# Optimization experiments

Measured on AMD Instinct MI355X. Metric: run time of the kernel, lower is better.

The kernel has to match this reference:

```python
import jax, jax.numpy as jnp
import numpy as np
from jax import lax

B, L = 16, 2048
D_TOK, D_TIS = 256, 64
D_MODEL = D_TOK + D_TIS          # 320
EXPAND = 2
D_INNER = EXPAND * D_MODEL       # 640
D_STATE = 16
D_CONV = 4
DT_RANK = (D_MODEL + 15) // 16   # 20 (ceil(d_model/16), Mamba default)
H_OUT = 128
VOCAB = 65                       # len(CODON_MAP_DNA)+1
N_TISSUES = 30
MAX_NORM = 2.0


def _embed_maxnorm(W, idx):
    # torch nn.Embedding(max_norm=2): looked-up rows are renormalized to norm<=2
    e = W[idx]
    n = jnp.linalg.norm(e, axis=-1, keepdims=True)
    return e * jnp.minimum(1.0, MAX_NORM / jnp.maximum(n, 1e-12))


def setup_inputs() -> dict:
    key = jax.random.key(0)
    ks = jax.random.split(key, 18)
    s = 0.02
    seq_W = jax.random.normal(ks[3], (VOCAB, D_TOK), dtype=jnp.float32)
    seq_W = seq_W.at[0].set(0.0)  # padding_idx=0
    A_log = jnp.log(jnp.broadcast_to(jnp.arange(1, D_STATE + 1, dtype=jnp.float32), (D_INNER, D_STATE)))
    return {
        "rna_data_pad": jax.random.randint(ks[0], (B, L), 0, VOCAB).astype(jnp.int32),
        "tissue_id": jax.random.randint(ks[1], (B,), 0, N_TISSUES).astype(jnp.int32),
        "seq_lengths": jax.random.randint(ks[2], (B,), 1, L + 1).astype(jnp.int32),
        "seq_W": seq_W,
        "tissue_W": jax.random.normal(ks[4], (N_TISSUES, D_TIS), dtype=jnp.float32),
        "in_proj_W": jax.random.normal(ks[5], (2 * D_INNER, D_MODEL), dtype=jnp.float32) * s,
        "conv_w": jax.random.normal(ks[6], (D_INNER, 1, D_CONV), dtype=jnp.float32) * s,
        "conv_b": jnp.zeros((D_INNER,), dtype=jnp.float32),
        "x_proj_W": jax.random.normal(ks[7], (DT_RANK + 2 * D_STATE, D_INNER), dtype=jnp.float32) * s,
        "dt_proj_W": jax.random.normal(ks[8], (D_INNER, DT_RANK), dtype=jnp.float32) * s,
        "dt_proj_b": jax.random.uniform(ks[9], (D_INNER,), minval=-4.0, maxval=-2.0),
        "A_log": A_log,
        "D_skip": jnp.ones((D_INNER,), dtype=jnp.float32),
        "out_proj_W": jax.random.normal(ks[10], (D_MODEL, D_INNER), dtype=jnp.float32) * s,
        "p1_W": jax.random.normal(ks[11], (H_OUT, D_MODEL), dtype=jnp.float32) * s,
        "p1_b": jnp.zeros((H_OUT,), dtype=jnp.float32),
        "p2_W": jax.random.normal(ks[12], (1, H_OUT), dtype=jnp.float32) * s,
        "p2_b": jnp.zeros((1,), dtype=jnp.float32),
    }


def reference(rna_data_pad, tissue_id, seq_lengths, seq_W, tissue_W, in_proj_W,
              conv_w, conv_b, x_proj_W, dt_proj_W, dt_proj_b, A_log, D_skip,
              out_proj_W, p1_W, p1_b, p2_W, p2_b):
    b, l = rna_data_pad.shape
    # embeddings + tissue broadcast + mask
    seq_emb = _embed_maxnorm(seq_W, rna_data_pad)            # [B,L,D_TOK]
    tis_emb = _embed_maxnorm(tissue_W, tissue_id)            # [B,D_TIS]
    tis_exp = jnp.broadcast_to(tis_emb[:, None, :], (b, l, tis_emb.shape[-1]))
    x = jnp.concatenate([seq_emb, tis_exp], axis=-1)          # [B,L,D_MODEL]
    x = x * (rna_data_pad != 0)[..., None]
    # Mamba block
    xz = x @ in_proj_W.T                                      # [B,L,2*D_INNER]
    xm, z = jnp.split(xz, 2, axis=-1)
    xt = xm.transpose(0, 2, 1)                                # [B,D_INNER,L]
    conv = lax.conv_general_dilated(
        xt, conv_w, window_strides=(1,), padding=[(D_CONV - 1, 0)],
        feature_group_count=D_INNER,
        dimension_numbers=("NCH", "OIH", "NCH")) + conv_b[None, :, None]
    xm = jax.nn.silu(conv).transpose(0, 2, 1)                 # [B,L,D_INNER]
    x_dbl = xm @ x_proj_W.T                                   # [B,L,DT_RANK+2*D_STATE]
    dt, Bm, Cm = jnp.split(x_dbl, [DT_RANK, DT_RANK + D_STATE], axis=-1)
    delta = jax.nn.softplus(dt @ dt_proj_W.T + dt_proj_b)     # [B,L,D_INNER]
    A = -jnp.exp(A_log)                                       # [D_INNER,D_STATE]
    # selective scan over time
    xs = (delta.transpose(1, 0, 2), Bm.transpose(1, 0, 2),
          Cm.transpose(1, 0, 2), xm.transpose(1, 0, 2))
    h0 = jnp.zeros((b, D_INNER, D_STATE), dtype=xm.dtype)

    def step(h, t):
        dl, bt, ct, ut = t                                    # [B,di],[B,ds],[B,ds],[B,di]
        dA = jnp.exp(dl[:, :, None] * A)                      # [B,di,ds]
        dBu = (dl * ut)[:, :, None] * bt[:, None, :]          # [B,di,ds]
        h = dA * h + dBu
        y = jnp.einsum("bds,bs->bd", h, ct)
        return h, y

    _, ys = lax.scan(step, h0, xs)                            # ys: [L,B,D_INNER]
    y = ys.transpose(1, 0, 2) + xm * D_skip
    y = y * jax.nn.silu(z)
    out = y @ out_proj_W.T                                    # [B,L,D_MODEL]
    # gather last valid timestep
    out_last = out[jnp.arange(b), seq_lengths - 1]            # [B,D_MODEL]
    h1 = jax.nn.relu(out_last @ p1_W.T + p1_b)
    return h1 @ p2_W.T + p2_b                                 # [B,1]
```

## Files before the change

### kernel.cpp

```cpp
#include <hip/hip_runtime.h>
#include <hip/hip_bf16.h>
#include <math.h>

#define B_      16
#define L_      2048
#define D_MODEL 320
#define D_INNER 640
#define D_STATE 16
#define DT_RANK 20
#define H_OUT   128
#define VOCAB   65
#define N_TIS   30
#define TT      8
#define ST      64
#define NCHUNK  16
#define CHLEN   (L_/NCHUNK)

static constexpr size_t OFF_MSEQ  = 0;
static constexpr size_t OFF_MTIS  = OFF_MSEQ + VOCAB*1280;
static constexpr size_t OFF_YSCAN = OFF_MTIS + N_TIS*1280;
static constexpr size_t OFF_CLAST = OFF_YSCAN + B_*D_INNER;
static constexpr size_t OFF_XD20  = OFF_CLAST + B_*16;
static constexpr size_t OFF_BBAR  = OFF_XD20 + (size_t)B_*L_*20;
static constexpr size_t OFF_PC    = OFF_BBAR + (size_t)B_*D_STATE*L_;
static constexpr size_t OFF_SC    = OFF_PC + (size_t)B_*NCHUNK*40*256;

__device__ __forceinline__ float fast_rcp(float x) { return __builtin_amdgcn_rcpf(x); }
__device__ __forceinline__ float silu_f(float x) { return x * fast_rcp(1.0f + __expf(-x)); }

__global__ __launch_bounds__(256) void k_mbuild(
    const float* __restrict__ seqW, const float* __restrict__ tisW,
    const float* __restrict__ inW, float* __restrict__ ws)
{
    __shared__ float a_l[256];
    __shared__ float red[4];
    int v = blockIdx.x, tid = threadIdx.x;
    int K, wofs; const float* src; float* dstM;
    if (v < VOCAB) { K = 256; wofs = 0;   src = seqW + (size_t)v*256;        dstM = ws + OFF_MSEQ + (size_t)v*1280; }
    else           { K = 64;  wofs = 256; src = tisW + (size_t)(v-VOCAB)*64; dstM = ws + OFF_MTIS + (size_t)(v-VOCAB)*1280; }
    float x = (tid < K) ? src[tid] : 0.0f;
    float ss = x * x;
    #pragma unroll
    for (int o = 32; o; o >>= 1) ss += __shfl_xor(ss, o);
    if ((tid & 63) == 0) red[tid >> 6] = ss;
    __syncthreads();
    float tot = red[0] + red[1] + red[2] + red[3];
    float scale = fminf(1.0f, 2.0f / fmaxf(sqrtf(tot), 1e-12f));
    a_l[tid] = (tid < K) ? x * scale : 0.0f;
    __syncthreads();

    int wv = tid >> 6, l = tid & 63;
    float4 a4 = ((const float4*)a_l)[l];
    int j0 = blockIdx.y * 256 + wv * 64;
    bool lane_on = (4*l < K);
    for (int jj = 0; jj < 64; jj += 4) {
        float p[4];
        #pragma unroll
        for (int u = 0; u < 4; ++u) {
            float pv = 0.0f;
            if (lane_on) {
                const float4 w4 = *(const float4*)(inW + (size_t)(j0 + jj + u)*320 + wofs + 4*l);
                pv = a4.x*w4.x + a4.y*w4.y + a4.z*w4.z + a4.w*w4.w;
            }
            p[u] = pv;
        }
        float ta, tb;
        ta=__shfl_xor(p[0],1); tb=__shfl_xor(p[1],1); p[0]=(l&1)?(p[1]+tb):(p[0]+ta);
        ta=__shfl_xor(p[2],1); tb=__shfl_xor(p[3],1); p[2]=(l&1)?(p[3]+tb):(p[2]+ta);
        ta=__shfl_xor(p[0],2); tb=__shfl_xor(p[2],2); p[0]=(l&2)?(p[2]+tb):(p[0]+ta);
        p[0]+=__shfl_xor(p[0],4);  p[0]+=__shfl_xor(p[0],8);
        p[0]+=__shfl_xor(p[0],16); p[0]+=__shfl_xor(p[0],32);
        if (l < 4) dstM[j0 + jj + l] = p[0];
    }
}

__global__ __launch_bounds__(256) void k_xdbl(
    const int* __restrict__ idx, const int* __restrict__ tissue_id,
    const int* __restrict__ seq_lengths,
    const float* __restrict__ conv_w, const float* __restrict__ conv_b,
    const float* __restrict__ xW, float* __restrict__ ws)
{
    __shared__ float u_l[TT*641];
    __shared__ float xd_l[TT*36];
    __shared__ int   idx_l[TT+3];
    int b = blockIdx.y;
    int t0 = blockIdx.x * TT;
    int t_last = seq_lengths[b] - 1;
    if (t0 > t_last) return;
    int tid = threadIdx.x;
    const float* Mseq = ws + OFF_MSEQ;
    const float* Mtis = ws + OFF_MTIS;
    int tis = tissue_id[b];
    if (tid < TT+3) {
        int t = t0 - 3 + tid;
        idx_l[tid] = (t >= 0) ? idx[b*L_ + t] : 0;
    }
    __syncthreads();

    for (int d = tid; d < D_INNER; d += 256) {
        float w0 = conv_w[d*4+0], w1 = conv_w[d*4+1], w2 = conv_w[d*4+2], w3 = conv_w[d*4+3];
        float cb = conv_b[d];
        float mt = Mtis[(size_t)tis*1280 + d];
        float xzv[TT+3];
        #pragma unroll
        for (int k = 0; k < TT+3; ++k) {
            unsigned ro = (unsigned)idx_l[k] * 1280u;
            xzv[k] = ro ? (Mseq[ro + (unsigned)d] + mt) : 0.0f;
        }
        #pragma unroll
        for (int t = 0; t < TT; ++t) {
            float c = cb;
            c = fmaf(w0, xzv[t+0], c);
            c = fmaf(w1, xzv[t+1], c);
            c = fmaf(w2, xzv[t+2], c);
            c = fmaf(w3, xzv[t+3], c);
            u_l[t*641 + d] = silu_f(c);
        }
    }
    __syncthreads();

    {
        int w = tid >> 6, l = tid & 63;
        float wreg[9][10];
        #pragma unroll
        for (int kk = 0; kk < 9; ++kk) {
            const float* xr = xW + (size_t)(w + 4*kk)*D_INNER + l;
            #pragma unroll
            for (int i = 0; i < 10; ++i) wreg[kk][i] = xr[64*i];
        }
        for (int t = 0; t < TT; ++t) {
            float p[9];
            #pragma unroll
            for (int kk = 0; kk < 9; ++kk) p[kk] = 0.f;
            #pragma unroll
            for (int i = 0; i < 10; ++i) {
                float ui = u_l[t*641 + l + 64*i];
                #pragma unroll
                for (int kk = 0; kk < 9; ++kk) p[kk] = fmaf(wreg[kk][i], ui, p[kk]);
            }
            {
                float ta, tb;
                ta=__shfl_xor(p[0],1); tb=__shfl_xor(p[1],1); p[0]=(l&1)?(p[1]+tb):(p[0]+ta);
                ta=__shfl_xor(p[2],1); tb=__shfl_xor(p[3],1); p[2]=(l&1)?(p[3]+tb):(p[2]+ta);
                ta=__shfl_xor(p[4],1); tb=__shfl_xor(p[5],1); p[4]=(l&1)?(p[5]+tb):(p[4]+ta);
                ta=__shfl_xor(p[6],1); tb=__shfl_xor(p[7],1); p[6]=(l&1)?(p[7]+tb):(p[6]+ta);
                p[8]+=__shfl_xor(p[8],1);
                ta=__shfl_xor(p[0],2); tb=__shfl_xor(p[2],2); p[0]=(l&2)?(p[2]+tb):(p[0]+ta);
                ta=__shfl_xor(p[4],2); tb=__shfl_xor(p[6],2); p[4]=(l&2)?(p[6]+tb):(p[4]+ta);
                p[8]+=__shfl_xor(p[8],2);
                ta=__shfl_xor(p[0],4); tb=__shfl_xor(p[4],4); p[0]=(l&4)?(p[4]+tb):(p[0]+ta);
                p[8]+=__shfl_xor(p[8],4);
                ta=__shfl_xor(p[0],8); tb=__shfl_xor(p[8],8); p[0]=(l&8)?(p[8]+tb):(p[0]+ta);
                p[0]+=__shfl_xor(p[0],16);
                p[0]+=__shfl_xor(p[0],32);
            }
            if (l < 9) xd_l[t*36 + w + 4*l] = p[0];
        }
        if (t_last < t0 + TT) {
            int tl = t_last - t0;
            float pc[4];
            #pragma unroll
            for (int k = 0; k < 4; ++k) pc[k] = 0.f;
            #pragma unroll
            for (int i = 0; i < 10; ++i) {
                float ui = u_l[tl*641 + l + 64*i];
                #pragma unroll
                for (int k = 0; k < 4; ++k)
                    pc[k] = fmaf(xW[(size_t)(36 + w + 4*k)*D_INNER + l + 64*i], ui, pc[k]);
            }
            #pragma unroll
            for (int o = 32; o; o >>= 1) {
                #pragma unroll
                for (int k = 0; k < 4; ++k) pc[k] += __shfl_xor(pc[k], o);
            }
            if (l == 0) {
                #pragma unroll
                for (int k = 0; k < 4; ++k) ws[OFF_CLAST + b*16 + w + 4*k] = pc[k];
            }
        }
    }
    __syncthreads();

    {
        int nt = min(TT, t_last - t0 + 1);
        int cnt = nt * 20;
        float* dst = ws + OFF_XD20 + ((size_t)b*L_ + t0)*20;
        for (int o = tid; o < cnt; o += 256) {
            int t = o / 20, r = o - t*20;
            dst[o] = xd_l[t*36 + r];
        }
        int cntB = nt * 16;
        if (tid < cntB) {
            int s, tt;
            if (nt == TT) { s = tid >> 3; tt = tid & 7; }
            else          { s = tid / nt; tt = tid - s*nt; }
            ws[OFF_BBAR + ((size_t)b*D_STATE + s)*L_ + t0 + tt] = xd_l[tt*36 + 20 + s];
        }
    }
}

__global__ __launch_bounds__(256) void k_scanc(
    const int* __restrict__ idx, const int* __restrict__ tissue_id,
    const int* __restrict__ seq_lengths,
    const float* __restrict__ conv_w, const float* __restrict__ conv_b,
    const float* __restrict__ dtW, const float* __restrict__ dtb,
    const float* __restrict__ A_log, float* __restrict__ ws)
{
    __shared__ float xd_t[ST*20];
    __shared__ float dl_t[16*68];
    __shared__ float du_t[16*68];
    __shared__ float Bb_t[16*68];
    __shared__ float sdred[16*17];
    __shared__ int   idx_t[ST+3];

    int dg = blockIdx.x, b = blockIdx.y, c = blockIdx.z;
    int t_last = seq_lengths[b] - 1;
    int t_begin = c * CHLEN;
    if (t_begin > t_last) return;
    int t_end = min(t_begin + CHLEN - 1, t_last);
    int tid = threadIdx.x;
    int dl = tid >> 4, s = tid & 15;
    int dd = tid & 15, tg = tid >> 4;
    int d_own = dg*16 + dd;
    unsigned dco = (unsigned)d_own;
    int tis = tissue_id[b];
    const float* Mseq = ws + OFF_MSEQ;

    float dtw_r[20];
    #pragma unroll
    for (int i = 0; i < 20; i += 4) {
        float4 w4 = *(const float4*)(dtW + d_own*20 + i);
        dtw_r[i] = w4.x; dtw_r[i+1] = w4.y; dtw_r[i+2] = w4.z; dtw_r[i+3] = w4.w;
    }
    float4 cw4 = *(const float4*)(conv_w + d_own*4);
    float  cb  = conv_b[d_own];
    float  dtb_v = dtb[d_own];
    float  mt  = ws[OFF_MTIS + (size_t)tis*1280 + d_own];
    float As = -__expf(A_log[(dg*16 + dl)*D_STATE + s]) * 1.44269504089f;

    float h = 0.0f;
    float sdp = 0.0f;
    for (int t0 = t_begin; t0 <= t_end; t0 += ST) {
        int nt = min(ST, t_end - t0 + 1);
        if (tid < ST+3) {
            int t = t0 - 3 + tid;
            idx_t[tid] = (t >= 0 && t < L_) ? idx[b*L_ + t] : 0;
        }
        {
            const float4* src = (const float4*)(ws + OFF_XD20 + ((size_t)b*L_ + t0)*20);
            float4* dst = (float4*)xd_t;
            int cnt4 = nt * 5;
            for (int o = tid; o < cnt4; o += 256) dst[o] = src[o];
        }
        {
            int lr = tid >> 4, c4 = (tid & 15) * 4;
            if (c4 < nt)
                *(float4*)(Bb_t + lr*68 + c4) =
                    *(const float4*)(ws + OFF_BBAR + ((size_t)b*D_STATE + lr)*L_ + t0 + c4);
        }
        __syncthreads();

        {
            int ttb = tg * 4;
            if (ttb < nt) {
                float xz[7];
                #pragma unroll
                for (int k = 0; k < 7; ++k) {
                    unsigned ro = (unsigned)idx_t[ttb + k] * 1280u;
                    xz[k] = ro ? (Mseq[ro + dco] + mt) : 0.0f;
                }
                float dl4[4], du4[4];
                bool full = (ttb + 3 < nt);
                #pragma unroll
                for (int j = 0; j < 4; ++j) {
                    int tt = ttb + j;
                    if (full || tt < nt) {
                        float cc = cb;
                        cc = fmaf(cw4.x, xz[j+0], cc);
                        cc = fmaf(cw4.y, xz[j+1], cc);
                        cc = fmaf(cw4.z, xz[j+2], cc);
                        cc = fmaf(cw4.w, xz[j+3], cc);
                        float u = silu_f(cc);
                        const float* xr = xd_t + tt*20;
                        float x = dtb_v;
                        #pragma unroll
                        for (int r = 0; r < 20; r += 4) {
                            float4 x4 = *(const float4*)(xr + r);
                            x = fmaf(x4.x, dtw_r[r+0], x);
                            x = fmaf(x4.y, dtw_r[r+1], x);
                            x = fmaf(x4.z, dtw_r[r+2], x);
                            x = fmaf(x4.w, dtw_r[r+3], x);
                        }
                        float e = __expf(-fabsf(x));
                        float sp = fmaxf(x, 0.0f) + __logf(1.0f + e);
                        dl4[j] = sp;
                        du4[j] = sp * u;
                        sdp += sp;
                    } else { dl4[j] = 0.f; du4[j] = 0.f; }
                }
                if (full) {
                    *(float4*)(dl_t + dd*68 + ttb) = make_float4(dl4[0], dl4[1], dl4[2], dl4[3]);
                    *(float4*)(du_t + dd*68 + ttb) = make_float4(du4[0], du4[1], du4[2], du4[3]);
                } else {
                    for (int j = 0; j < 4 && ttb + j < nt; ++j) {
                        dl_t[dd*68 + ttb + j] = dl4[j];
                        du_t[dd*68 + ttb + j] = du4[j];
                    }
                }
            }
        }
        __syncthreads();

        {
            int q4 = nt >> 2;
            #pragma unroll 8
            for (int q = 0; q < q4; ++q) {
                float4 d4 = *(const float4*)(dl_t + dl*68 + 4*q);
                float4 u4 = *(const float4*)(du_t + dl*68 + 4*q);
                float4 b4 = *(const float4*)(Bb_t + s*68 + 4*q);
                float e0 = exp2f(d4.x*As), e1 = exp2f(d4.y*As);
                float e2 = exp2f(d4.z*As), e3 = exp2f(d4.w*As);
                float c0 = u4.x*b4.x, c1 = u4.y*b4.y;
                float c2 = u4.z*b4.z, c3 = u4.w*b4.w;
                h = fmaf(e0, h, c0); h = fmaf(e1, h, c1);
                h = fmaf(e2, h, c2); h = fmaf(e3, h, c3);
            }
            for (int tt = q4*4; tt < nt; ++tt) {
                float dlt = dl_t[dl*68 + tt];
                h = fmaf(exp2f(dlt * As), h, du_t[dl*68 + tt] * Bb_t[s*68 + tt]);
            }
        }
        __syncthreads();
    }
    sdred[tg*17 + dd] = sdp;
    __syncthreads();
    float sd = 0.0f;
    #pragma unroll
    for (int g = 0; g < 16; ++g) sd += sdred[g*17 + dl];
    float P = exp2f(As * sd);
    size_t base = (((size_t)b*NCHUNK + c)*40 + dg)*256 + tid;
    ws[OFF_PC + base] = P;
    ws[OFF_SC + base] = h;
}

__global__ __launch_bounds__(256) void k_comb(const int* __restrict__ seq_lengths,
                                              float* __restrict__ ws)
{
    int b = blockIdx.y, dg = blockIdx.x;
    int tid = threadIdx.x;
    int dl = tid >> 4, s = tid & 15;
    int t_last = seq_lengths[b] - 1;
    int ncv = t_last / CHLEN + 1;
    float h = 0.0f;
    for (int c = 0; c < ncv; ++c) {
        size_t base = (((size_t)b*NCHUNK + c)*40 + dg)*256 + tid;
        h = fmaf(ws[OFF_PC + base], h, ws[OFF_SC + base]);
    }
    float v = h * ws[OFF_CLAST + b*16 + s];
    v += __shfl_xor(v, 1); v += __shfl_xor(v, 2);
    v += __shfl_xor(v, 4); v += __shfl_xor(v, 8);
    if (s == 0) ws[OFF_YSCAN + (size_t)b*D_INNER + dg*16 + dl] = v;
}

__global__ __launch_bounds__(320) void k_final(
    const int* __restrict__ idx, const int* __restrict__ tissue_id,
    const int* __restrict__ seq_lengths,
    const float* __restrict__ conv_w, const float* __restrict__ conv_b,
    const float* __restrict__ Dskip, const float* __restrict__ outW,
    const float* __restrict__ p1W, const float* __restrict__ p1b,
    const float* __restrict__ p2W, const float* __restrict__ p2b,
    const float* __restrict__ ws, float* __restrict__ out)
{
    __shared__ float y_l[D_INNER];
    __shared__ float o_l[D_MODEL];
    __shared__ float h1_l[H_OUT];
    int b = blockIdx.x, tid = threadIdx.x;
    int t_last = seq_lengths[b] - 1;
    int tis = tissue_id[b];
    const float* Mseq = ws + OFF_MSEQ;
    const float* Mtis = ws + OFF_MTIS;
    int rows[4];
    #pragma unroll
    for (int k = 0; k < 4; ++k) {
        int t = t_last - 3 + k;
        rows[k] = (t >= 0) ? idx[b*L_ + t] : 0;
    }
    for (int d = tid; d < D_INNER; d += 320) {
        float conv = conv_b[d];
        const float* cw = conv_w + d*4;
        #pragma unroll
        for (int k = 0; k < 4; ++k) {
            unsigned ro = (unsigned)rows[k] * 1280u;
            float xzv = ro ? (Mseq[ro + (unsigned)d] + Mtis[(size_t)tis*1280 + d]) : 0.0f;
            conv += cw[k] * xzv;
        }
        float u = silu_f(conv);
        unsigned roL = (unsigned)rows[3] * 1280u;
        float z = roL ? (Mseq[roL + 640u + (unsigned)d] + Mtis[(size_t)tis*1280 + 640 + d]) : 0.0f;
        float ys = ws[OFF_YSCAN + (size_t)b*D_INNER + d];
        y_l[d] = (ys + u * Dskip[d]) * silu_f(z);
    }
    __syncthreads();
    if (tid < D_MODEL) {
        const float* w = outW + tid*D_INNER;
        float acc = 0.f;
        #pragma unroll 4
        for (int k = 0; k < D_INNER; k += 4) {
            float4 w4 = *(const float4*)(w + k);
            acc += y_l[k]*w4.x + y_l[k+1]*w4.y + y_l[k+2]*w4.z + y_l[k+3]*w4.w;
        }
        o_l[tid] = acc;
    }
    __syncthreads();
    if (tid < H_OUT) {
        const float* w = p1W + tid*D_MODEL;
        float acc = p1b[tid];
        #pragma unroll 4
        for (int k = 0; k < D_MODEL; k += 4) {
            float4 w4 = *(const float4*)(w + k);
            acc += o_l[k]*w4.x + o_l[k+1]*w4.y + o_l[k+2]*w4.z + o_l[k+3]*w4.w;
        }
        h1_l[tid] = fmaxf(acc, 0.0f);
    }
    __syncthreads();
    if (tid == 0) {
        float acc = p2b[0];
        for (int k = 0; k < H_OUT; ++k) acc += h1_l[k]*p2W[k];
        out[b] = acc;
    }
}

extern "C" void kernel_launch(void* const* d_in, const int* in_sizes, int n_in,
                              void* d_out, int out_size, void* d_ws, size_t ws_size,
                              hipStream_t stream)
{
    const int*   idx   = (const int*)d_in[0];
    const int*   tis   = (const int*)d_in[1];
    const int*   slen  = (const int*)d_in[2];
    const float* seqW  = (const float*)d_in[3];
    const float* tisW  = (const float*)d_in[4];
    const float* inW   = (const float*)d_in[5];
    const float* convw = (const float*)d_in[6];
    const float* convb = (const float*)d_in[7];
    const float* xW    = (const float*)d_in[8];
    const float* dtW   = (const float*)d_in[9];
    const float* dtb   = (const float*)d_in[10];
    const float* Alog  = (const float*)d_in[11];
    const float* Dsk   = (const float*)d_in[12];
    const float* outW  = (const float*)d_in[13];
    const float* p1W   = (const float*)d_in[14];
    const float* p1b   = (const float*)d_in[15];
    const float* p2W   = (const float*)d_in[16];
    const float* p2b   = (const float*)d_in[17];
    float* ws  = (float*)d_ws;
    float* out = (float*)d_out;

    hipLaunchKernelGGL(k_mbuild, dim3(VOCAB + N_TIS, 5), dim3(256), 0, stream, seqW, tisW, inW, ws);
    hipLaunchKernelGGL(k_xdbl,   dim3(L_/TT, B_),        dim3(256), 0, stream,
                       idx, tis, slen, convw, convb, xW, ws);
    hipLaunchKernelGGL(k_scanc,  dim3(D_INNER/16, B_, NCHUNK), dim3(256), 0, stream,
                       idx, tis, slen, convw, convb, dtW, dtb, Alog, ws);
    hipLaunchKernelGGL(k_comb,   dim3(D_INNER/16, B_),   dim3(256), 0, stream, slen, ws);
    hipLaunchKernelGGL(k_final,  dim3(B_),               dim3(320), 0, stream,
                       idx, tis, slen, convw, convb, Dsk, outW, p1W, p1b, p2W, p2b, ws, out);
}
```

Measured before the change: 250.0 us.

## Cache conv+SiLU output in fp16 workspace for scan; widen final MLP kernel

k_xdbl now writes the post-conv SiLU activation u to a new fp16 workspace buffer, and k_scanc reads it back instead of re-gathering embedding rows and recomputing the depthwise conv and SiLU. This is enabled only when the workspace is large enough, so the old recompute path stays as a fallback. k_final is relaunched with 1024 threads and splits the dot products across lanes with shuffle reductions, shortening its serial per-thread loops. The cost is an extra B*L*640 half-precision write and read, plus fp16 rounding of u.

```diff
diff --git a/kernel.cpp b/kernel.cpp
--- a/kernel.cpp
+++ b/kernel.cpp
@@ -1,5 +1,6 @@
 #include <hip/hip_runtime.h>
 #include <hip/hip_bf16.h>
+#include <hip/hip_fp16.h>
 #include <math.h>
 
 #define B_      16
@@ -24,6 +25,8 @@
 static constexpr size_t OFF_BBAR  = OFF_XD20 + (size_t)B_*L_*20;
 static constexpr size_t OFF_PC    = OFF_BBAR + (size_t)B_*D_STATE*L_;
 static constexpr size_t OFF_SC    = OFF_PC + (size_t)B_*NCHUNK*40*256;
+static constexpr size_t OFF_U     = OFF_SC + (size_t)B_*NCHUNK*40*256;
+static constexpr size_t WS_NEED_BYTES = OFF_U*4 + (size_t)B_*L_*D_INNER*2;
 
 __device__ __forceinline__ float fast_rcp(float x) { return __builtin_amdgcn_rcpf(x); }
 __device__ __forceinline__ float silu_f(float x) { return x * fast_rcp(1.0f + __expf(-x)); }
@@ -78,7 +81,7 @@
     const int* __restrict__ idx, const int* __restrict__ tissue_id,
     const int* __restrict__ seq_lengths,
     const float* __restrict__ conv_w, const float* __restrict__ conv_b,
-    const float* __restrict__ xW, float* __restrict__ ws)
+    const float* __restrict__ xW, float* __restrict__ ws, int use_u)
 {
     __shared__ float u_l[TT*641];
     __shared__ float xd_l[TT*36];
@@ -119,6 +122,16 @@
     }
     __syncthreads();
 
+    if (use_u) {
+        int nt = min(TT, t_last - t0 + 1);
+        __half* Ub = (__half*)(ws + OFF_U) + ((size_t)b*L_ + t0)*D_INNER;
+        int cnt = nt * D_INNER;
+        for (int o = tid; o < cnt; o += 256) {
+            int t = o / D_INNER, d = o - t*D_INNER;
+            Ub[o] = __float2half(u_l[t*641 + d]);
+        }
+    }
+
     {
         int w = tid >> 6, l = tid & 63;
         float wreg[9][10];
@@ -204,7 +217,7 @@
     const int* __restrict__ seq_lengths,
     const float* __restrict__ conv_w, const float* __restrict__ conv_b,
     const float* __restrict__ dtW, const float* __restrict__ dtb,
-    const float* __restrict__ A_log, float* __restrict__ ws)
+    const float* __restrict__ A_log, float* __restrict__ ws, int use_u)
 {
     __shared__ float xd_t[ST*20];
     __shared__ float dl_t[16*68];
@@ -232,17 +245,21 @@
         float4 w4 = *(const float4*)(dtW + d_own*20 + i);
         dtw_r[i] = w4.x; dtw_r[i+1] = w4.y; dtw_r[i+2] = w4.z; dtw_r[i+3] = w4.w;
     }
-    float4 cw4 = *(const float4*)(conv_w + d_own*4);
-    float  cb  = conv_b[d_own];
+    float4 cw4 = make_float4(0.f,0.f,0.f,0.f);
+    float  cb = 0.f, mt = 0.f;
+    if (!use_u) {
+        cw4 = *(const float4*)(conv_w + d_own*4);
+        cb  = conv_b[d_own];
+        mt  = ws[OFF_MTIS + (size_t)tis*1280 + d_own];
+    }
     float  dtb_v = dtb[d_own];
-    float  mt  = ws[OFF_MTIS + (size_t)tis*1280 + d_own];
     float As = -__expf(A_log[(dg*16 + dl)*D_STATE + s]) * 1.44269504089f;
 
     float h = 0.0f;
     float sdp = 0.0f;
     for (int t0 = t_begin; t0 <= t_end; t0 += ST) {
         int nt = min(ST, t_end - t0 + 1);
-        if (tid < ST+3) {
+        if (!use_u && tid < ST+3) {
             int t = t0 - 3 + tid;
             idx_t[tid] = (t >= 0 && t < L_) ? idx[b*L_ + t] : 0;
         }
@@ -263,11 +280,29 @@
         {
             int ttb = tg * 4;
             if (ttb < nt) {
-                float xz[7];
-                #pragma unroll
-                for (int k = 0; k < 7; ++k) {
-                    unsigned ro = (unsigned)idx_t[ttb + k] * 1280u;
-                    xz[k] = ro ? (Mseq[ro + dco] + mt) : 0.0f;
+                float uu[4];
+                if (use_u) {
+                    const __half* Ub = (const __half*)(ws + OFF_U)
+                                     + ((size_t)b*L_ + t0 + ttb)*D_INNER + dco;
+                    #pragma unroll
+                    for (int j = 0; j < 4; ++j)
+                        uu[j] = (ttb + j < nt) ? __half2float(Ub[(size_t)j*D_INNER]) : 0.0f;
+                } else {
+                    float xz[7];
+                    #pragma unroll
+                    for (int k = 0; k < 7; ++k) {
+                        unsigned ro = (unsigned)idx_t[ttb + k] * 1280u;
+                        xz[k] = ro ? (Mseq[ro + dco] + mt) : 0.0f;
+                    }
+                    #pragma unroll
+                    for (int j = 0; j < 4; ++j) {
+                        float cc = cb;
+                        cc = fmaf(cw4.x, xz[j+0], cc);
+                        cc = fmaf(cw4.y, xz[j+1], cc);
+                        cc = fmaf(cw4.z, xz[j+2], cc);
+                        cc = fmaf(cw4.w, xz[j+3], cc);
+                        uu[j] = (ttb + j < nt) ? silu_f(cc) : 0.0f;
+                    }
                 }
                 float dl4[4], du4[4];
                 bool full = (ttb + 3 < nt);
@@ -275,12 +310,6 @@
                 for (int j = 0; j < 4; ++j) {
                     int tt = ttb + j;
                     if (full || tt < nt) {
-                        float cc = cb;
-                        cc = fmaf(cw4.x, xz[j+0], cc);
-                        cc = fmaf(cw4.y, xz[j+1], cc);
-                        cc = fmaf(cw4.z, xz[j+2], cc);
-                        cc = fmaf(cw4.w, xz[j+3], cc);
-                        float u = silu_f(cc);
                         const float* xr = xd_t + tt*20;
                         float x = dtb_v;
                         #pragma unroll
@@ -294,7 +323,7 @@
                         float e = __expf(-fabsf(x));
                         float sp = fmaxf(x, 0.0f) + __logf(1.0f + e);
                         dl4[j] = sp;
-                        du4[j] = sp * u;
+                        du4[j] = sp * uu[j];
                         sdp += sp;
                     } else { dl4[j] = 0.f; du4[j] = 0.f; }
                 }
@@ -362,7 +391,7 @@
     if (s == 0) ws[OFF_YSCAN + (size_t)b*D_INNER + dg*16 + dl] = v;
 }
 
-__global__ __launch_bounds__(320) void k_final(
+__global__ __launch_bounds__(1024) void k_final(
     const int* __restrict__ idx, const int* __restrict__ tissue_id,
     const int* __restrict__ seq_lengths,
     const float* __restrict__ conv_w, const float* __restrict__ conv_b,
@@ -385,7 +414,8 @@
         int t = t_last - 3 + k;
         rows[k] = (t >= 0) ? idx[b*L_ + t] : 0;
     }
-    for (int d = tid; d < D_INNER; d += 320) {
+    if (tid < D_INNER) {
+        int d = tid;
         float conv = conv_b[d];
         const float* cw = conv_w + d*4;
         #pragma unroll
@@ -401,32 +431,43 @@
         y_l[d] = (ys + u * Dskip[d]) * silu_f(z);
     }
     __syncthreads();
-    if (tid < D_MODEL) {
-        const float* w = outW + tid*D_INNER;
+    {
+        int j = tid >> 1, half = tid & 1;
         float acc = 0.f;
-        #pragma unroll 4
-        for (int k = 0; k < D_INNER; k += 4) {
-            float4 w4 = *(const float4*)(w + k);
-            acc += y_l[k]*w4.x + y_l[k+1]*w4.y + y_l[k+2]*w4.z + y_l[k+3]*w4.w;
-        }
-        o_l[tid] = acc;
-    }
-    __syncthreads();
-    if (tid < H_OUT) {
-        const float* w = p1W + tid*D_MODEL;
-        float acc = p1b[tid];
-        #pragma unroll 4
-        for (int k = 0; k < D_MODEL; k += 4) {
-            float4 w4 = *(const float4*)(w + k);
-            acc += o_l[k]*w4.x + o_l[k+1]*w4.y + o_l[k+2]*w4.z + o_l[k+3]*w4.w;
-        }
-        h1_l[tid] = fmaxf(acc, 0.0f);
-    }
-    __syncthreads();
-    if (tid == 0) {
-        float acc = p2b[0];
-        for (int k = 0; k < H_OUT; ++k) acc += h1_l[k]*p2W[k];
-        out[b] = acc;
+        if (j < D_MODEL) {
+            const float* w = outW + (size_t)j*D_INNER + half*320;
+            const float* y = y_l + half*320;
+            #pragma unroll 4
+            for (int k = 0; k < 320; k += 4) {
+                float4 w4 = *(const float4*)(w + k);
+                acc += y[k]*w4.x + y[k+1]*w4.y + y[k+2]*w4.z + y[k+3]*w4.w;
+            }
+        }
+        acc += __shfl_xor(acc, 1);
+        if (j < D_MODEL && half == 0) o_l[j] = acc;
+    }
+    __syncthreads();
+    {
+        int j = tid >> 3, part = tid & 7;
+        float acc = 0.f;
+        if (j < H_OUT) {
+            const float* w = p1W + (size_t)j*D_MODEL + part*40;
+            const float* o = o_l + part*40;
+            #pragma unroll
+            for (int k = 0; k < 40; k += 4) {
+                float4 w4 = *(const float4*)(w + k);
+                acc += o[k]*w4.x + o[k+1]*w4.y + o[k+2]*w4.z + o[k+3]*w4.w;
+            }
+        }
+        acc += __shfl_xor(acc, 1); acc += __shfl_xor(acc, 2); acc += __shfl_xor(acc, 4);
+        if (j < H_OUT && part == 0) h1_l[j] = fmaxf(acc + p1b[j], 0.0f);
+    }
+    __syncthreads();
+    if (tid < 64) {
+        float v = h1_l[tid]*p2W[tid] + h1_l[tid+64]*p2W[tid+64];
+        v += __shfl_xor(v, 32); v += __shfl_xor(v, 16); v += __shfl_xor(v, 8);
+        v += __shfl_xor(v, 4);  v += __shfl_xor(v, 2);  v += __shfl_xor(v, 1);
+        if (tid == 0) out[b] = v + p2b[0];
     }
 }
 
@@ -455,12 +496,14 @@
     float* ws  = (float*)d_ws;
     float* out = (float*)d_out;
 
+    int use_u = (ws_size >= WS_NEED_BYTES) ? 1 : 0;
+
     hipLaunchKernelGGL(k_mbuild, dim3(VOCAB + N_TIS, 5), dim3(256), 0, stream, seqW, tisW, inW, ws);
     hipLaunchKernelGGL(k_xdbl,   dim3(L_/TT, B_),        dim3(256), 0, stream,
-                       idx, tis, slen, convw, convb, xW, ws);
+                       idx, tis, slen, convw, convb, xW, ws, use_u);
     hipLaunchKernelGGL(k_scanc,  dim3(D_INNER/16, B_, NCHUNK), dim3(256), 0, stream,
-                       idx, tis, slen, convw, convb, dtW, dtb, Alog, ws);
+                       idx, tis, slen, convw, convb, dtW, dtb, Alog, ws, use_u);
     hipLaunchKernelGGL(k_comb,   dim3(D_INNER/16, B_),   dim3(256), 0, stream, slen, ws);
-    hipLaunchKernelGGL(k_final,  dim3(B_),               dim3(320), 0, stream,
+    hipLaunchKernelGGL(k_final,  dim3(B_),               dim3(1024), 0, stream,
                        idx, tis, slen, convw, convb, Dsk, outW, p1W, p1b, p2W, p2b, ws, out);
 }
```

Result: faster. 244.8 us (-2.1%).
